# Optimization experiments

Hardware: AMD Instinct MI355X
Metric: run time of the kernel (lower is better)

Reference implementation:

```python
import jax, jax.numpy as jnp
import numpy as np

N_NODES = 100000


def setup_inputs() -> dict:
    key = jax.random.key(0)
    k1, k2, k3, k4, k5 = jax.random.split(key, 5)
    d_in, d_out, n_edges = 128, 128, 640000
    x = jax.random.normal(k1, (N_NODES, d_in), dtype=jnp.float32)
    edge_index = jax.random.randint(k2, (2, n_edges), 0, N_NODES, dtype=jnp.int64)
    # uniform(size, W) in the source is U(-1/sqrt(in), 1/sqrt(in)); scaled normal is fine as data
    s = 1.0 / np.sqrt(d_in)
    Wc = jax.random.normal(k3, (d_in, d_out), dtype=jnp.float32) * s
    Wn = jax.random.normal(k4, (d_in, d_out), dtype=jnp.float32) * s
    b = jax.random.normal(k5, (d_out,), dtype=jnp.float32) * s
    return {"x": x, "edge_index": edge_index, "Wc": Wc, "Wn": Wn, "b": b}


def reference(x, edge_index, Wc, Wn, b):
    row, col = edge_index[0], edge_index[1]
    alpha = x @ Wc                      # [N, out]
    beta = x @ Wn                       # [N, out]
    # Vectorized scatter-mean replacing the original per-node Python loop:
    # gamma[n] = mean(beta[col[row == n]])
    num = jax.ops.segment_sum(beta[col], row, num_segments=N_NODES)   # [N, out]
    cnt = jax.ops.segment_sum(jnp.ones_like(row, dtype=beta.dtype), row, num_segments=N_NODES)
    gamma = num / jnp.maximum(cnt, 1.0)[:, None]  # NOTE: unused below, exactly as in the original forward
    del gamma
    # The original returns alpha + beta + bias (gamma is dead code in the source).
    return alpha + beta + b
```

## Files before the change

kernel.cpp:

```cpp
#include <hip/hip_runtime.h>
#include <hip/hip_bf16.h>


#define NROWS 100000

typedef __attribute__((ext_vector_type(8))) __bf16 bf16x8;
typedef __attribute__((ext_vector_type(8))) unsigned short u16x8;
typedef __attribute__((ext_vector_type(4))) float f32x4;

__device__ __forceinline__ unsigned short f2bf(float f) {
    unsigned int u = __builtin_bit_cast(unsigned int, f);
    u += 0x7FFFu + ((u >> 16) & 1u);
    return (unsigned short)(u >> 16);
}

__device__ __forceinline__ bf16x8 pack8(const float4 lo, const float4 hi) {
    u16x8 r;
    r[0] = f2bf(lo.x); r[1] = f2bf(lo.y); r[2] = f2bf(lo.z); r[3] = f2bf(lo.w);
    r[4] = f2bf(hi.x); r[5] = f2bf(hi.y); r[6] = f2bf(hi.z); r[7] = f2bf(hi.w);
    return __builtin_bit_cast(bf16x8, r);
}

__global__ void prep_wt(const float* __restrict__ Wc, const float* __restrict__ Wn,
                        unsigned short* __restrict__ wt) {
    int i = blockIdx.x * 256 + threadIdx.x;
    int n = i >> 7, k = i & 127;
    wt[i] = f2bf(Wc[k * 128 + n] + Wn[k * 128 + n]);
}

__global__ __launch_bounds__(256) void gemm_bias(
    const float* __restrict__ x, const unsigned short* __restrict__ wt,
    const float* __restrict__ bias_g, float* __restrict__ out) {

    __shared__ __align__(16) unsigned short sWt[128 * 136];

    const int tid = threadIdx.x;
    #pragma unroll
    for (int it = 0; it < 8; ++it) {
        int idx8 = it * 256 + tid;
        int n = idx8 >> 4;
        int k = (idx8 & 15) << 3;
        *(u16x8*)&sWt[n * 136 + k] = *(const u16x8*)(wt + (idx8 << 3));
    }
    __syncthreads();

    const int wave = tid >> 6;
    const int lane = tid & 63;
    const int quad = lane >> 4;
    const int l16  = lane & 15;

    const long rowbase = (long)blockIdx.x * 128 + wave * 32;
    if (rowbase >= NROWS) return;

    float bv[8];
    #pragma unroll
    for (int ct = 0; ct < 8; ++ct) bv[ct] = bias_g[ct * 16 + l16];

    f32x4 acc[2][8] = {};

    const float* xr0 = x + (rowbase + l16) * 128;
    const float* xr1 = xr0 + 16 * 128;

    #pragma unroll
    for (int kc = 0; kc < 4; ++kc) {
        const int ko = kc * 32 + quad * 8;
        float4 a0lo = *(const float4*)(xr0 + ko);
        float4 a0hi = *(const float4*)(xr0 + ko + 4);
        float4 a1lo = *(const float4*)(xr1 + ko);
        float4 a1hi = *(const float4*)(xr1 + ko + 4);
        bf16x8 a0 = pack8(a0lo, a0hi);
        bf16x8 a1 = pack8(a1lo, a1hi);
        #pragma unroll
        for (int ct = 0; ct < 8; ++ct) {
            bf16x8 bf = *(const bf16x8*)&sWt[(ct * 16 + l16) * 136 + ko];
            acc[0][ct] = __builtin_amdgcn_mfma_f32_16x16x32_bf16(a0, bf, acc[0][ct], 0, 0, 0);
            acc[1][ct] = __builtin_amdgcn_mfma_f32_16x16x32_bf16(a1, bf, acc[1][ct], 0, 0, 0);
        }
    }

    #pragma unroll
    for (int mt = 0; mt < 2; ++mt) {
        #pragma unroll
        for (int r = 0; r < 4; ++r) {
            float* orow = out + (rowbase + mt * 16 + quad * 4 + r) * 128;
            #pragma unroll
            for (int ct = 0; ct < 8; ++ct) {
                orow[ct * 16 + l16] = acc[mt][ct][r] + bv[ct];
            }
        }
    }
}

extern "C" void kernel_launch(void* const* d_in, const int* in_sizes, int n_in,
                              void* d_out, int out_size, void* d_ws, size_t ws_size,
                              hipStream_t stream) {
    const float* x  = (const float*)d_in[0];
    const float* Wc = (const float*)d_in[2];
    const float* Wn = (const float*)d_in[3];
    const float* b  = (const float*)d_in[4];
    unsigned short* wt = (unsigned short*)d_ws;
    float* out = (float*)d_out;

    prep_wt<<<64, 256, 0, stream>>>(Wc, Wn, wt);
    const int nblocks = (NROWS + 127) / 128;
    gemm_bias<<<nblocks, 256, 0, stream>>>(x, wt, b, out);
}
```

Before: 112.6 us.

## Fuse weight prep into GEMM and swap MFMA operands for float4 output stores

Removes the separate weight-prep kernel launch: each block now reads Wc and Wn itself, sums them, converts to bf16 and writes a transposed copy into shared memory using a staggered write order meant to reduce bank conflicts. The MFMA operand order is swapped so that each lane holds four consecutive output columns of one row, which lets the epilogue issue float4 stores and float4 bias loads instead of scalar ones. The cost is that every block repeats the weight transform (more global reads of Wc/Wn and scalar LDS writes) in exchange for saving a launch and getting wider output stores.

```diff
diff --git a/kernel.cpp b/kernel.cpp
--- a/kernel.cpp
+++ b/kernel.cpp
@@ -1,5 +1,4 @@
 #include <hip/hip_runtime.h>
-#include <hip/hip_bf16.h>
 
 
 #define NROWS 100000
@@ -21,40 +20,50 @@
     return __builtin_bit_cast(bf16x8, r);
 }
 
-__global__ void prep_wt(const float* __restrict__ Wc, const float* __restrict__ Wn,
-                        unsigned short* __restrict__ wt) {
-    int i = blockIdx.x * 256 + threadIdx.x;
-    int n = i >> 7, k = i & 127;
-    wt[i] = f2bf(Wc[k * 128 + n] + Wn[k * 128 + n]);
-}
-
 __global__ __launch_bounds__(256) void gemm_bias(
-    const float* __restrict__ x, const unsigned short* __restrict__ wt,
-    const float* __restrict__ bias_g, float* __restrict__ out) {
+    const float* __restrict__ x, const float* __restrict__ Wc,
+    const float* __restrict__ Wn, const float* __restrict__ bias_g,
+    float* __restrict__ out) {
 
     __shared__ __align__(16) unsigned short sWt[128 * 136];
 
-    const int tid = threadIdx.x;
-    #pragma unroll
-    for (int it = 0; it < 8; ++it) {
-        int idx8 = it * 256 + tid;
-        int n = idx8 >> 4;
-        int k = (idx8 & 15) << 3;
-        *(u16x8*)&sWt[n * 136 + k] = *(const u16x8*)(wt + (idx8 << 3));
+    const int tid  = threadIdx.x;
+    const int wave = tid >> 6;
+    const int lane = tid & 63;
+
+    {
+        const int nb = (lane & 7) + 8 * wave;
+        const int kb = lane >> 3;
+        const int st = (lane >> 1) & 3;
+        #pragma unroll
+        for (int it = 0; it < 16; ++it) {
+            const int k = it * 8 + kb;
+            const float4 c4 = *(const float4*)(Wc + k * 128 + nb * 4);
+            const float4 n4 = *(const float4*)(Wn + k * 128 + nb * 4);
+            unsigned short b4[4];
+            b4[0] = f2bf(c4.x + n4.x);
+            b4[1] = f2bf(c4.y + n4.y);
+            b4[2] = f2bf(c4.z + n4.z);
+            b4[3] = f2bf(c4.w + n4.w);
+            #pragma unroll
+            for (int d = 0; d < 4; ++d) {
+                const int dp = (d + st) & 3;
+                sWt[(nb * 4 + dp) * 136 + k] = b4[dp];
+            }
+        }
     }
     __syncthreads();
 
-    const int wave = tid >> 6;
-    const int lane = tid & 63;
     const int quad = lane >> 4;
     const int l16  = lane & 15;
 
     const long rowbase = (long)blockIdx.x * 128 + wave * 32;
     if (rowbase >= NROWS) return;
 
-    float bv[8];
+    float4 bv[8];
     #pragma unroll
-    for (int ct = 0; ct < 8; ++ct) bv[ct] = bias_g[ct * 16 + l16];
+    for (int ct = 0; ct < 8; ++ct)
+        bv[ct] = *(const float4*)(bias_g + ct * 16 + quad * 4);
 
     f32x4 acc[2][8] = {};
 
@@ -72,21 +81,23 @@
         bf16x8 a1 = pack8(a1lo, a1hi);
         #pragma unroll
         for (int ct = 0; ct < 8; ++ct) {
-            bf16x8 bf = *(const bf16x8*)&sWt[(ct * 16 + l16) * 136 + ko];
-            acc[0][ct] = __builtin_amdgcn_mfma_f32_16x16x32_bf16(a0, bf, acc[0][ct], 0, 0, 0);
-            acc[1][ct] = __builtin_amdgcn_mfma_f32_16x16x32_bf16(a1, bf, acc[1][ct], 0, 0, 0);
+            bf16x8 wf = *(const bf16x8*)&sWt[(ct * 16 + l16) * 136 + ko];
+            acc[0][ct] = __builtin_amdgcn_mfma_f32_16x16x32_bf16(wf, a0, acc[0][ct], 0, 0, 0);
+            acc[1][ct] = __builtin_amdgcn_mfma_f32_16x16x32_bf16(wf, a1, acc[1][ct], 0, 0, 0);
         }
     }
 
     #pragma unroll
     for (int mt = 0; mt < 2; ++mt) {
+        float* orow = out + (rowbase + mt * 16 + l16) * 128;
         #pragma unroll
-        for (int r = 0; r < 4; ++r) {
-            float* orow = out + (rowbase + mt * 16 + quad * 4 + r) * 128;
-            #pragma unroll
-            for (int ct = 0; ct < 8; ++ct) {
-                orow[ct * 16 + l16] = acc[mt][ct][r] + bv[ct];
-            }
+        for (int ct = 0; ct < 8; ++ct) {
+            float4 st4;
+            st4.x = acc[mt][ct][0] + bv[ct].x;
+            st4.y = acc[mt][ct][1] + bv[ct].y;
+            st4.z = acc[mt][ct][2] + bv[ct].z;
+            st4.w = acc[mt][ct][3] + bv[ct].w;
+            *(float4*)(orow + ct * 16 + quad * 4) = st4;
         }
     }
 }
@@ -98,10 +109,9 @@
     const float* Wc = (const float*)d_in[2];
     const float* Wn = (const float*)d_in[3];
     const float* b  = (const float*)d_in[4];
-    unsigned short* wt = (unsigned short*)d_ws;
     float* out = (float*)d_out;
+    (void)d_ws; (void)ws_size;
 
-    prep_wt<<<64, 256, 0, stream>>>(Wc, Wn, wt);
     const int nblocks = (NROWS + 127) / 128;
-    gemm_bias<<<nblocks, 256, 0, stream>>>(x, wt, b, out);
+    gemm_bias<<<nblocks, 256, 0, stream>>>(x, Wc, Wn, b, out);
 }
```

Result: slower. 118.5 us (+5.2%).
